# Optimization experiments

Hardware: AMD Instinct MI355X
Metric: run time of the kernel (lower is better)

## Reference

```python
import jax, jax.numpy as jnp
import numpy as np

BN_EPS = 1e-5

def setup_inputs() -> dict:
    key = jax.random.key(0)
    ks = jax.random.split(key, 7)
    B, D, A = 16384, 768, 51
    s = 1.0 / np.sqrt(D)
    return {
        "x": jax.random.normal(ks[0], (B, D), dtype=jnp.float32),
        "W_embed": jax.random.uniform(ks[1], (D, D), minval=-s, maxval=s, dtype=jnp.float32),
        "b_embed": jax.random.uniform(ks[2], (D,), minval=-s, maxval=s, dtype=jnp.float32),
        "W_attr": jax.random.uniform(ks[3], (A, D), minval=-s, maxval=s, dtype=jnp.float32),  # stacked per-attribute (dim->1) heads
        "b_attr": jax.random.uniform(ks[4], (A,), minval=-s, maxval=s, dtype=jnp.float32),
        "gamma": jnp.ones((A,), dtype=jnp.float32),
        "beta": jnp.zeros((A,), dtype=jnp.float32),
    }

def reference(x, W_embed, b_embed, W_attr, b_attr, gamma, beta):
    # word_embed: Linear(dim, dim)
    h = x @ W_embed.T + b_embed                      # [B, D]
    # fused per-attribute heads: cat of attr_num (dim->1) linears == one (dim->attr_num) matmul
    logits = h @ W_attr.T + b_attr                    # [B, A]
    # BatchNorm1d (training mode: batch statistics, biased variance)
    mean = jnp.mean(logits, axis=0)
    var = jnp.var(logits, axis=0)
    y = (logits - mean) * jax.lax.rsqrt(var + BN_EPS) * gamma + beta
    return y
```

## Files before the change

### kernel.cpp

```cpp
#include <hip/hip_runtime.h>

typedef _Float16 halfx8 __attribute__((ext_vector_type(8)));
typedef float floatx4 __attribute__((ext_vector_type(4)));
typedef float floatx2 __attribute__((ext_vector_type(2)));

#define GLOBAL_AS __attribute__((address_space(1)))
#define LDS_AS __attribute__((address_space(3)))

__device__ __forceinline__ void async_copy_16(const void* g, void* l) {
    __builtin_amdgcn_global_load_lds((GLOBAL_AS void*)g, (LDS_AS void*)l, 16, 0, 0);
}

#define PM 16384
#define PD 768
#define PA 51
#define NBLK 256u


__device__ __forceinline__ size_t fragidx(int a, int d) {
    return (size_t)(d >> 5) * 2048 + (size_t)(a >> 4) * 512
         + (size_t)((a & 15) | (((d >> 3) & 3) << 4)) * 8 + (d & 7);
}

__global__ __launch_bounds__(256) void prep_kernel(
    const float* __restrict__ We, const float* __restrict__ be,
    const float* __restrict__ Wa, const float* __restrict__ ba,
    _Float16* __restrict__ wfrag, float* __restrict__ bc,
    unsigned int* __restrict__ counter)
{
    const int wave = threadIdx.x >> 6;
    const int lane = threadIdx.x & 63;
    const int Wu = __builtin_amdgcn_readfirstlane((int)blockIdx.x * 4 + wave);

    if (Wu < 312) {
        const int pair = Wu / 12;
        const int dchunk = Wu - pair * 12;
        const int a0 = pair * 2;
        const bool has1 = (a0 + 1 < PA);
        const int d = dchunk * 64 + lane;
        const float* wa0 = Wa + (size_t)a0 * PD;
        const float* wa1 = Wa + (size_t)(has1 ? a0 + 1 : a0) * PD;
        float acc0 = 0.f, acc1 = 0.f;
        #pragma unroll 32
        for (int k = 0; k < PD; ++k) {
            float w = We[(size_t)k * PD + d];
            acc0 = fmaf(w, wa0[k], acc0);
            acc1 = fmaf(w, wa1[k], acc1);
        }
        wfrag[fragidx(a0, d)] = (_Float16)acc0;
        if (has1) wfrag[fragidx(a0 + 1, d)] = (_Float16)acc1;
    } else if (Wu < 325) {
        const int r = PA + (Wu - 312);
        #pragma unroll
        for (int j = 0; j < 12; ++j)
            wfrag[fragidx(r, j * 64 + lane)] = (_Float16)0.f;
    } else if (Wu < 376) {
        const int a = Wu - 325;
        float p = 0.f;
        #pragma unroll
        for (int j = 0; j < 12; ++j) {
            int k = j * 64 + lane;
            p = fmaf(Wa[(size_t)a * PD + k], be[k], p);
        }
        #pragma unroll
        for (int off = 32; off; off >>= 1) p += __shfl_down(p, off);
        if (lane == 0) bc[a] = p + ba[a];
    } else if (Wu == 376) {
        if (lane == 0) *counter = 0u;
    }
}

__global__ void __launch_bounds__(256, 1) gemm_kernel(
    const float* __restrict__ X,
    const _Float16* __restrict__ Wfrag,
    const float* __restrict__ bc,
    const float* __restrict__ gamma,
    const float* __restrict__ beta,
    float* __restrict__ logits,
    unsigned long long* __restrict__ part,
    unsigned int* __restrict__ counter,
    float* __restrict__ ss)
{
    __shared__ __attribute__((aligned(16))) _Float16 Bh[24 * 4 * 512];
    __shared__ __attribute__((aligned(16))) float Atile[4][3][16 * 64];
    __shared__ float s_sum[64];
    __shared__ float s_ssq[64];
    __shared__ float redS[256];
    __shared__ float redQ[256];
    __shared__ int s_last;

    const int tid = threadIdx.x;
    const int wave = tid >> 6;
    const int lane = tid & 63;
    const int quad = lane >> 4;
    const int l16 = lane & 15;
    const int m0 = (int)blockIdx.x * 64 + wave * 16;

    if (tid < 64) { s_sum[tid] = 0.f; s_ssq[tid] = 0.f; }

    #pragma unroll
    for (int j = 0; j < 24; ++j) {
        int ch = wave * 24 + j;
        async_copy_16((const char*)Wfrag + (size_t)ch * 1024 + (size_t)lane * 16,
                      (char*)Bh + (size_t)ch * 1024);
    }
    asm volatile("" ::: "memory");

    auto stageA = [&](int buf, int kt) {
        #pragma unroll
        for (int j = 0; j < 4; ++j) {
            int r = j * 4 + (lane >> 4);
            int c = lane & 15;
            int csw = (c & 8) | ((c & 7) ^ (r & 7));
            async_copy_16(X + (size_t)(m0 + r) * PD + kt + csw * 4,
                          (char*)&Atile[wave][buf][0] + (size_t)(j * 64) * 16);
        }
        asm volatile("" ::: "memory");
    };

    floatx4 acc[4];
    #pragma unroll
    for (int n = 0; n < 4; ++n) acc[n] = (floatx4){0.f, 0.f, 0.f, 0.f};

    stageA(0, 0);
    stageA(1, 64);
    stageA(2, 128);
    asm volatile("s_waitcnt vmcnt(12)\n\ts_barrier" ::: "memory");

    #pragma unroll
    for (int mm = 0; mm < 12; ++mm) {
        if (mm <= 9)       asm volatile("s_waitcnt vmcnt(8)" ::: "memory");
        else if (mm == 10) asm volatile("s_waitcnt vmcnt(4)" ::: "memory");
        else               asm volatile("s_waitcnt vmcnt(0)" ::: "memory");
        const float* At = &Atile[wave][mm % 3][0];
        #pragma unroll
        for (int km = 0; km < 2; ++km) {
            const int ks = mm * 2 + km;
            int cc = km * 8 + quad * 2;
            int s3 = l16 & 7;
            floatx4 p0 = *(const floatx4*)&At[l16 * 64 + (((cc & 8) | ((cc & 7) ^ s3)) << 2)];
            floatx4 p1 = *(const floatx4*)&At[l16 * 64 + ((((cc + 1) & 8) | (((cc + 1) & 7) ^ s3)) << 2)];
            halfx8 af;
            af[0] = (_Float16)p0[0]; af[1] = (_Float16)p0[1];
            af[2] = (_Float16)p0[2]; af[3] = (_Float16)p0[3];
            af[4] = (_Float16)p1[0]; af[5] = (_Float16)p1[1];
            af[6] = (_Float16)p1[2]; af[7] = (_Float16)p1[3];
            #pragma unroll
            for (int n = 0; n < 4; ++n) {
                halfx8 bf = *(const halfx8*)&Bh[(size_t)(ks * 4 + n) * 512 + (size_t)lane * 8];
                acc[n] = __builtin_amdgcn_mfma_f32_16x16x32_f16(af, bf, acc[n], 0, 0, 0);
            }
        }
        if (mm + 3 < 12) stageA(mm % 3, (mm + 3) * 64);
    }

    #pragma unroll
    for (int n = 0; n < 4; ++n) {
        int col = n * 16 + l16;
        if (col < PA) {
            float bv = bc[col];
            float ps = 0.f, pss = 0.f;
            int rowb = m0 + quad * 4;
            #pragma unroll
            for (int r = 0; r < 4; ++r) {
                float v = acc[n][r] + bv;
                logits[(size_t)(rowb + r) * PA + col] = v;
                ps += v; pss += v * v;
            }
            atomicAdd(&s_sum[col], ps);
            atomicAdd(&s_ssq[col], pss);
        }
    }
    __syncthreads();

    if (tid < 64) {
        union { floatx2 f; unsigned long long u; } v;
        v.f = (floatx2){s_sum[tid], s_ssq[tid]};
        __hip_atomic_store(&part[(size_t)blockIdx.x * 64 + tid], v.u,
                           __ATOMIC_RELAXED, __HIP_MEMORY_SCOPE_AGENT);
    }
    __syncthreads();

    if (tid == 0) {
        unsigned int old = __hip_atomic_fetch_add(counter, 1u, __ATOMIC_ACQ_REL,
                                                  __HIP_MEMORY_SCOPE_AGENT);
        s_last = (old == NBLK - 1u);
    }
    __syncthreads();
    if (s_last) {
        const int col = tid & 63;
        const int q = tid >> 6;
        float rs = 0.f, rq = 0.f;
        #pragma unroll 8
        for (int i = q * 64; i < q * 64 + 64; ++i) {
            union { unsigned long long u; floatx2 f; } v;
            v.u = __hip_atomic_load(&part[(size_t)i * 64 + col],
                                    __ATOMIC_RELAXED, __HIP_MEMORY_SCOPE_AGENT);
            rs += v.f[0]; rq += v.f[1];
        }
        redS[tid] = rs; redQ[tid] = rq;
        __syncthreads();
        const float invB = 1.0f / (float)PM;
        if (tid < PA) {
            float s  = redS[tid] + redS[64 + tid] + redS[128 + tid] + redS[192 + tid];
            float sq = redQ[tid] + redQ[64 + tid] + redQ[128 + tid] + redQ[192 + tid];
            float mean = s * invB;
            float var  = sq * invB - mean * mean;
            float inv  = rsqrtf(var + 1e-5f);
            float sc = gamma[tid] * inv;
            ss[tid] = sc;
            ss[64 + tid] = beta[tid] - mean * sc;
        }
    }
}

__global__ __launch_bounds__(256) void bn_kernel(
    const float* __restrict__ logits,
    const float* __restrict__ ss,
    float* __restrict__ out)
{
    __shared__ float sc[64];
    __shared__ float sh[64];
    const int t = threadIdx.x;
    if (t < 64) { sc[t] = ss[t]; sh[t] = ss[64 + t]; }
    __syncthreads();

    const int idx = (int)blockIdx.x * 256 + t;
    floatx4 v = ((const floatx4*)logits)[idx];
    int c0 = (idx * 4) % 51;
    int c1 = c0 + 1; if (c1 >= 51) c1 -= 51;
    int c2 = c1 + 1; if (c2 >= 51) c2 -= 51;
    int c3 = c2 + 1; if (c3 >= 51) c3 -= 51;
    floatx4 r;
    r[0] = v[0] * sc[c0] + sh[c0];
    r[1] = v[1] * sc[c1] + sh[c1];
    r[2] = v[2] * sc[c2] + sh[c2];
    r[3] = v[3] * sc[c3] + sh[c3];
    ((floatx4*)out)[idx] = r;
}

extern "C" void kernel_launch(void* const* d_in, const int* in_sizes, int n_in,
                              void* d_out, int out_size, void* d_ws, size_t ws_size,
                              hipStream_t stream) {
    const float* x       = (const float*)d_in[0];
    const float* W_embed = (const float*)d_in[1];
    const float* b_embed = (const float*)d_in[2];
    const float* W_attr  = (const float*)d_in[3];
    const float* b_attr  = (const float*)d_in[4];
    const float* gamma   = (const float*)d_in[5];
    const float* beta    = (const float*)d_in[6];
    float* out = (float*)d_out;

    char* ws = (char*)d_ws;
    _Float16* wfrag       = (_Float16*)(ws);
    float* bc             = (float*)(ws + 98304);
    unsigned int* counter = (unsigned int*)(ws + 98560);
    unsigned long long* part = (unsigned long long*)(ws + 98816);
    float* ssbuf          = (float*)(ws + 229888);
    float* logits         = (float*)(ws + 230400);

    prep_kernel<<<95, 256, 0, stream>>>(W_embed, b_embed, W_attr, b_attr,
                                        wfrag, bc, counter);
    gemm_kernel<<<256, 256, 0, stream>>>(x, wfrag, bc, gamma, beta,
                                         logits, part, counter, ssbuf);
    bn_kernel<<<816, 256, 0, stream>>>(logits, ssbuf, out);
}
```

Measured before the change: 141.6 us.

## Split K across waves with 1024 small blocks and LDS atomic reduction

Replaces the LDS-staged, async-copy pipelined GEMM, where each block handled 64 rows, with 1024 blocks of 16 rows. Each wave now covers a quarter of the K dimension, reading X and the fp16 weight fragments directly from global memory, and the waves combine partial sums through LDS atomics. This aims to raise occupancy and parallelism by launching four times as many blocks with no large LDS footprint. In exchange it loses LDS reuse of the weight fragments, which are now reloaded from global or L2 by every block, and the final statistics reduction has to sum four times as many partials.

```diff
diff --git a/kernel.cpp b/kernel.cpp
--- a/kernel.cpp
+++ b/kernel.cpp
@@ -4,17 +4,10 @@
 typedef float floatx4 __attribute__((ext_vector_type(4)));
 typedef float floatx2 __attribute__((ext_vector_type(2)));
 
-#define GLOBAL_AS __attribute__((address_space(1)))
-#define LDS_AS __attribute__((address_space(3)))
-
-__device__ __forceinline__ void async_copy_16(const void* g, void* l) {
-    __builtin_amdgcn_global_load_lds((GLOBAL_AS void*)g, (LDS_AS void*)l, 16, 0, 0);
-}
-
 #define PM 16384
 #define PD 768
 #define PA 51
-#define NBLK 256u
+#define NBLK 1024u
 
 
 __device__ __forceinline__ size_t fragidx(int a, int d) {
@@ -70,7 +63,7 @@
     }
 }
 
-__global__ void __launch_bounds__(256, 1) gemm_kernel(
+__global__ void __launch_bounds__(256, 4) gemm_kernel(
     const float* __restrict__ X,
     const _Float16* __restrict__ Wfrag,
     const float* __restrict__ bc,
@@ -81,8 +74,7 @@
     unsigned int* __restrict__ counter,
     float* __restrict__ ss)
 {
-    __shared__ __attribute__((aligned(16))) _Float16 Bh[24 * 4 * 512];
-    __shared__ __attribute__((aligned(16))) float Atile[4][3][16 * 64];
+    __shared__ float s_out[16][64];
     __shared__ float s_sum[64];
     __shared__ float s_ssq[64];
     __shared__ float redS[256];
@@ -94,77 +86,53 @@
     const int lane = tid & 63;
     const int quad = lane >> 4;
     const int l16 = lane & 15;
-    const int m0 = (int)blockIdx.x * 64 + wave * 16;
-
+    const int b = (int)blockIdx.x;
+
+    #pragma unroll
+    for (int i = 0; i < 4; ++i) ((float*)s_out)[i * 256 + tid] = 0.f;
     if (tid < 64) { s_sum[tid] = 0.f; s_ssq[tid] = 0.f; }
-
-    #pragma unroll
-    for (int j = 0; j < 24; ++j) {
-        int ch = wave * 24 + j;
-        async_copy_16((const char*)Wfrag + (size_t)ch * 1024 + (size_t)lane * 16,
-                      (char*)Bh + (size_t)ch * 1024);
-    }
-    asm volatile("" ::: "memory");
-
-    auto stageA = [&](int buf, int kt) {
-        #pragma unroll
-        for (int j = 0; j < 4; ++j) {
-            int r = j * 4 + (lane >> 4);
-            int c = lane & 15;
-            int csw = (c & 8) | ((c & 7) ^ (r & 7));
-            async_copy_16(X + (size_t)(m0 + r) * PD + kt + csw * 4,
-                          (char*)&Atile[wave][buf][0] + (size_t)(j * 64) * 16);
-        }
-        asm volatile("" ::: "memory");
-    };
+    __syncthreads();
 
     floatx4 acc[4];
     #pragma unroll
     for (int n = 0; n < 4; ++n) acc[n] = (floatx4){0.f, 0.f, 0.f, 0.f};
 
-    stageA(0, 0);
-    stageA(1, 64);
-    stageA(2, 128);
-    asm volatile("s_waitcnt vmcnt(12)\n\ts_barrier" ::: "memory");
-
-    #pragma unroll
-    for (int mm = 0; mm < 12; ++mm) {
-        if (mm <= 9)       asm volatile("s_waitcnt vmcnt(8)" ::: "memory");
-        else if (mm == 10) asm volatile("s_waitcnt vmcnt(4)" ::: "memory");
-        else               asm volatile("s_waitcnt vmcnt(0)" ::: "memory");
-        const float* At = &Atile[wave][mm % 3][0];
-        #pragma unroll
-        for (int km = 0; km < 2; ++km) {
-            const int ks = mm * 2 + km;
-            int cc = km * 8 + quad * 2;
-            int s3 = l16 & 7;
-            floatx4 p0 = *(const floatx4*)&At[l16 * 64 + (((cc & 8) | ((cc & 7) ^ s3)) << 2)];
-            floatx4 p1 = *(const floatx4*)&At[l16 * 64 + ((((cc + 1) & 8) | (((cc + 1) & 7) ^ s3)) << 2)];
-            halfx8 af;
-            af[0] = (_Float16)p0[0]; af[1] = (_Float16)p0[1];
-            af[2] = (_Float16)p0[2]; af[3] = (_Float16)p0[3];
-            af[4] = (_Float16)p1[0]; af[5] = (_Float16)p1[1];
-            af[6] = (_Float16)p1[2]; af[7] = (_Float16)p1[3];
-            #pragma unroll
-            for (int n = 0; n < 4; ++n) {
-                halfx8 bf = *(const halfx8*)&Bh[(size_t)(ks * 4 + n) * 512 + (size_t)lane * 8];
-                acc[n] = __builtin_amdgcn_mfma_f32_16x16x32_f16(af, bf, acc[n], 0, 0, 0);
-            }
-        }
-        if (mm + 3 < 12) stageA(mm % 3, (mm + 3) * 64);
-    }
-
-    #pragma unroll
-    for (int n = 0; n < 4; ++n) {
-        int col = n * 16 + l16;
+    const float* xrow = X + (size_t)(b * 16 + l16) * PD + wave * 192 + quad * 8;
+    const _Float16* bbase = Wfrag + (size_t)(wave * 6) * 2048 + (size_t)lane * 8;
+
+    #pragma unroll
+    for (int s = 0; s < 6; ++s) {
+        floatx4 p0 = *(const floatx4*)(xrow + s * 32);
+        floatx4 p1 = *(const floatx4*)(xrow + s * 32 + 4);
+        halfx8 af;
+        af[0] = (_Float16)p0[0]; af[1] = (_Float16)p0[1];
+        af[2] = (_Float16)p0[2]; af[3] = (_Float16)p0[3];
+        af[4] = (_Float16)p1[0]; af[5] = (_Float16)p1[1];
+        af[6] = (_Float16)p1[2]; af[7] = (_Float16)p1[3];
+        #pragma unroll
+        for (int n = 0; n < 4; ++n) {
+            halfx8 bf = *(const halfx8*)(bbase + (size_t)(s * 4 + n) * 512);
+            acc[n] = __builtin_amdgcn_mfma_f32_16x16x32_f16(af, bf, acc[n], 0, 0, 0);
+        }
+    }
+
+    #pragma unroll
+    for (int n = 0; n < 4; ++n)
+        #pragma unroll
+        for (int r = 0; r < 4; ++r)
+            atomicAdd(&s_out[quad * 4 + r][n * 16 + l16], acc[n][r]);
+    __syncthreads();
+
+    {
+        const int col = tid & 63;
+        const int rg = tid >> 6;
         if (col < PA) {
             float bv = bc[col];
             float ps = 0.f, pss = 0.f;
-            int rowb = m0 + quad * 4;
             #pragma unroll
             for (int r = 0; r < 4; ++r) {
-                float v = acc[n][r] + bv;
-                logits[(size_t)(rowb + r) * PA + col] = v;
+                float v = s_out[rg * 4 + r][col] + bv;
+                logits[(size_t)(b * 16 + rg * 4 + r) * PA + col] = v;
                 ps += v; pss += v * v;
             }
             atomicAdd(&s_sum[col], ps);
@@ -176,7 +144,7 @@
     if (tid < 64) {
         union { floatx2 f; unsigned long long u; } v;
         v.f = (floatx2){s_sum[tid], s_ssq[tid]};
-        __hip_atomic_store(&part[(size_t)blockIdx.x * 64 + tid], v.u,
+        __hip_atomic_store(&part[(size_t)b * 64 + tid], v.u,
                            __ATOMIC_RELAXED, __HIP_MEMORY_SCOPE_AGENT);
     }
     __syncthreads();
@@ -192,7 +160,7 @@
         const int q = tid >> 6;
         float rs = 0.f, rq = 0.f;
         #pragma unroll 8
-        for (int i = q * 64; i < q * 64 + 64; ++i) {
+        for (int i = q * 256; i < q * 256 + 256; ++i) {
             union { unsigned long long u; floatx2 f; } v;
             v.u = __hip_atomic_load(&part[(size_t)i * 64 + col],
                                     __ATOMIC_RELAXED, __HIP_MEMORY_SCOPE_AGENT);
@@ -256,12 +224,12 @@
     float* bc             = (float*)(ws + 98304);
     unsigned int* counter = (unsigned int*)(ws + 98560);
     unsigned long long* part = (unsigned long long*)(ws + 98816);
-    float* ssbuf          = (float*)(ws + 229888);
-    float* logits         = (float*)(ws + 230400);
+    float* ssbuf          = (float*)(ws + 623104);
+    float* logits         = (float*)(ws + 623616);
 
     prep_kernel<<<95, 256, 0, stream>>>(W_embed, b_embed, W_attr, b_attr,
                                         wfrag, bc, counter);
-    gemm_kernel<<<256, 256, 0, stream>>>(x, wfrag, bc, gamma, beta,
-                                         logits, part, counter, ssbuf);
+    gemm_kernel<<<1024, 256, 0, stream>>>(x, wfrag, bc, gamma, beta,
+                                          logits, part, counter, ssbuf);
     bn_kernel<<<816, 256, 0, stream>>>(logits, ssbuf, out);
 }
```

Result: slower. 175.3 us (+23.8%).
